# Kernel optimization log

Hardware: AMD Instinct MI355X
Metric: run time of the kernel (lower is better)

Reference implementation:

```python
import jax, jax.numpy as jnp
import numpy as np

B, T, D, NH = 4, 2048, 768, 12
DH = D // NH
NEG = -100000.0  # module uses masked_fill with -100000.0, not -inf


def setup_inputs() -> dict:
    key = jax.random.key(0)
    ks = jax.random.split(key, 9)
    s = 1.0 / np.sqrt(D)
    return {
        "x": jax.random.normal(ks[0], (B, T, D), jnp.float32),
        "wq": jax.random.normal(ks[1], (D, D), jnp.float32) * s,
        "bq": jax.random.normal(ks[2], (D,), jnp.float32) * 0.02,
        "wk": jax.random.normal(ks[3], (D, D), jnp.float32) * s,
        "bk": jax.random.normal(ks[4], (D,), jnp.float32) * 0.02,
        "wv": jax.random.normal(ks[5], (D, D), jnp.float32) * s,
        "bv": jax.random.normal(ks[6], (D,), jnp.float32) * 0.02,
        "wo": jax.random.normal(ks[7], (D, D), jnp.float32) * s,
        "bo": jax.random.normal(ks[8], (D,), jnp.float32) * 0.02,
    }


def reference(x, wq, bq, wk, bk, wv, bv, wo, bo):
    Bx, Tx, E = x.shape
    # torch Linear: y = x @ W.T + b, weight shape [out, in]
    def heads(w, b):
        return (x @ w.T + b).reshape(Bx, Tx, NH, DH).transpose(0, 2, 1, 3)  # [B,nh,T,dh]
    Q, K, V = heads(wq, bq), heads(wk, bk), heads(wv, bv)
    scale = 1.0 / jnp.sqrt(jnp.float32(DH))
    QK = jnp.einsum("bhqd,bhkd->bhqk", Q, K) * scale  # [B,nh,T,T]
    causal = jnp.tril(jnp.ones((Tx, Tx), dtype=bool))
    QK = jnp.where(causal, QK, NEG)
    A = jax.nn.softmax(QK, axis=-1)  # attn_dropout p=0 (eval)
    Z = jnp.einsum("bhqk,bhkd->bhqd", A, V)
    Z = Z.transpose(0, 2, 1, 3).reshape(Bx, Tx, E)
    return Z @ wo.T + bo  # resid_dropout p=0 (eval)
```

## Files before the change

kernel.cpp:

```cpp
#include <hip/hip_runtime.h>


#define B_ 4
#define T_ 2048
#define D_ 768
#define NH_ 12
#define DH_ 64
#define M_ (B_ * T_)

typedef __attribute__((ext_vector_type(8))) short bf16x8;
typedef __attribute__((ext_vector_type(4))) float f32x4;

__device__ __forceinline__ unsigned short f2bf(float f) {
  unsigned int u = __builtin_bit_cast(unsigned int, f);
  u += 0x7FFFu + ((u >> 16) & 1u);
  return (unsigned short)(u >> 16);
}

__device__ __forceinline__ void async16(const void* g, void* l) {
  __builtin_amdgcn_global_load_lds(
      (const __attribute__((address_space(1))) unsigned int*)g,
      (__attribute__((address_space(3))) unsigned int*)l, 16, 0, 0);
}

__global__ void cvt_kernel(const float* __restrict__ x, const float* __restrict__ wq,
                           const float* __restrict__ wk, const float* __restrict__ wv,
                           const float* __restrict__ wo,
                           unsigned short* __restrict__ xb, unsigned short* __restrict__ wqb,
                           unsigned short* __restrict__ wkb, unsigned short* __restrict__ wvb,
                           unsigned short* __restrict__ wob) {
  const float* src; unsigned short* dst; int n4;
  switch (blockIdx.y) {
    case 0: src = x;  dst = xb;  n4 = M_ * D_ / 4; break;
    case 1: src = wq; dst = wqb; n4 = D_ * D_ / 4; break;
    case 2: src = wk; dst = wkb; n4 = D_ * D_ / 4; break;
    case 3: src = wv; dst = wvb; n4 = D_ * D_ / 4; break;
    default: src = wo; dst = wob; n4 = D_ * D_ / 4; break;
  }
  int stride = gridDim.x * blockDim.x;
  for (int i = blockIdx.x * blockDim.x + threadIdx.x; i < n4; i += stride) {
    float4 v = ((const float4*)src)[i];
    ushort4 o;
    o.x = f2bf(v.x); o.y = f2bf(v.y); o.z = f2bf(v.z); o.w = f2bf(v.w);
    ((ushort4*)dst)[i] = o;
  }
}

__global__ __launch_bounds__(256) void gemm_kernel(
    const unsigned short* __restrict__ A,
    const unsigned short* __restrict__ W0, const unsigned short* __restrict__ W1,
    const unsigned short* __restrict__ W2,
    const float* __restrict__ bias0, const float* __restrict__ bias1,
    const float* __restrict__ bias2,
    void* out0, void* out1, void* out2,
    float s0, float s1, float s2,
    int M, int N, int K, int qkv) {
  __shared__ __align__(16) unsigned short As[2][128 * 64];
  __shared__ __align__(16) unsigned short Bs[2][128 * 64];

  int bid = blockIdx.x;
  int xcd = bid & 7, g = bid >> 3;
  int mt, nt, y;
  if (qkv) { mt = xcd + ((g / 18) << 3); int sub = g % 18; y = sub / 6; nt = sub % 6; }
  else     { mt = xcd + ((g / 6) << 3);  nt = g % 6; y = 0; }

  const unsigned short* W = y == 0 ? W0 : (y == 1 ? W1 : W2);
  const float* bias = y == 0 ? bias0 : (y == 1 ? bias1 : bias2);
  void* outp = y == 0 ? out0 : (y == 1 ? out1 : out2);
  float scl = y == 0 ? s0 : (y == 1 ? s1 : s2);
  int mode = qkv ? ((y == 2) ? 2 : 1) : 0;

  int tid = threadIdx.x, lane = tid & 63, w = tid >> 6;
  int l15 = lane & 15, l4 = lane >> 4;
  int wr = w >> 1, wc = w & 1;

  int m0 = mt << 7;
  int n0 = nt << 7;

  f32x4 acc[4][4] = {};

  int sRow[4], sCol[4];
#pragma unroll
  for (int c = 0; c < 4; ++c) {
    int pos = ((c * 4 + w) * 64 + lane) * 8;
    int row = pos >> 6, colE = pos & 63;
    sRow[c] = row;
    sCol[c] = colE ^ ((row & 7) << 3);
  }

#pragma unroll
  for (int c = 0; c < 4; ++c) {
    async16(A + (size_t)(m0 + sRow[c]) * K + sCol[c], (char*)As[0] + (c * 4 + w) * 1024);
    async16(W + (size_t)(n0 + sRow[c]) * K + sCol[c], (char*)Bs[0] + (c * 4 + w) * 1024);
  }

  int nkt = K >> 6;
#pragma unroll 1
  for (int t = 0; t < nkt; ++t) {
    int cur = t & 1;
    __syncthreads();
    if (t + 1 < nkt) {
      int kt1 = (t + 1) << 6;
#pragma unroll
      for (int c = 0; c < 4; ++c) {
        async16(A + (size_t)(m0 + sRow[c]) * K + kt1 + sCol[c],
                (char*)As[cur ^ 1] + (c * 4 + w) * 1024);
        async16(W + (size_t)(n0 + sRow[c]) * K + kt1 + sCol[c],
                (char*)Bs[cur ^ 1] + (c * 4 + w) * 1024);
      }
    }
#pragma unroll
    for (int ks = 0; ks < 2; ++ks) {
      bf16x8 af[4], bfr[4];
#pragma unroll
      for (int m = 0; m < 4; ++m) {
        int row = wr * 64 + m * 16 + l15;
        int cb = (ks * 64 + l4 * 16) ^ ((row & 7) << 4);
        af[m] = *(const bf16x8*)((const char*)As[cur] + row * 128 + cb);
      }
#pragma unroll
      for (int n = 0; n < 4; ++n) {
        int row = wc * 64 + n * 16 + l15;
        int cb = (ks * 64 + l4 * 16) ^ ((row & 7) << 4);
        bfr[n] = *(const bf16x8*)((const char*)Bs[cur] + row * 128 + cb);
      }
#pragma unroll
      for (int m = 0; m < 4; ++m)
#pragma unroll
        for (int n = 0; n < 4; ++n)
          acc[m][n] = __builtin_amdgcn_mfma_f32_16x16x32_bf16(af[m], bfr[n], acc[m][n], 0, 0, 0);
    }
  }

  if (mode == 2) {
#pragma unroll
    for (int n = 0; n < 4; ++n) {
      int col = n0 + wc * 64 + n * 16 + l15;
      float bv = bias[col];
      int h = col >> 6, d = col & 63;
#pragma unroll
      for (int m = 0; m < 4; ++m) {
        int rbase = m0 + wr * 64 + m * 16 + l4 * 4;
        int bb = rbase >> 11, t = rbase & (T_ - 1);
        ushort4 o;
        o.x = f2bf(acc[m][n][0] + bv);
        o.y = f2bf(acc[m][n][1] + bv);
        o.z = f2bf(acc[m][n][2] + bv);
        o.w = f2bf(acc[m][n][3] + bv);
        *(ushort4*)((unsigned short*)outp + ((size_t)(bb * NH_ + h) * DH_ + d) * T_ + t) = o;
      }
    }
  } else {
#pragma unroll
    for (int n = 0; n < 4; ++n) {
      int col = n0 + wc * 64 + n * 16 + l15;
      float bv = bias[col];
#pragma unroll
      for (int m = 0; m < 4; ++m) {
        int rbase = m0 + wr * 64 + m * 16 + l4 * 4;
#pragma unroll
        for (int r = 0; r < 4; ++r) {
          float v = (acc[m][n][r] + bv) * scl;
          size_t idx = (size_t)(rbase + r) * N + col;
          if (mode == 1) ((unsigned short*)outp)[idx] = f2bf(v);
          else           ((float*)outp)[idx] = v;
        }
      }
    }
  }
}

__global__ __launch_bounds__(256, 3) void attn_kernel(
    const unsigned short* __restrict__ Q, const unsigned short* __restrict__ Kg,
    const unsigned short* __restrict__ VT, unsigned short* __restrict__ Z) {
  __shared__ __align__(16) char lds[41984];

  int tid = threadIdx.x, lane = tid & 63, w = tid >> 6;
  int l15 = lane & 15, l4 = lane >> 4;
  int bid = blockIdx.x;
  int xcd = bid & 7, g = bid >> 3;
  int bh = xcd + ((g >> 4) << 3);
  int pr = g & 15;
  int b = bh / NH_, h = bh % NH_;

  const unsigned short* Qb = Q + (size_t)(b * T_) * D_ + h * DH_;
  const unsigned short* Kb = Kg + (size_t)(b * T_) * D_ + h * DH_;
  const unsigned short* VTb = VT + (size_t)(b * NH_ + h) * DH_ * T_;

  int sRow[2], sCol[2];
#pragma unroll
  for (int c = 0; c < 2; ++c) {
    int pos = ((c * 4 + w) * 64 + lane) * 8;
    int row = pos >> 6, colE = pos & 63;
    sRow[c] = row;
    sCol[c] = colE ^ ((row & 7) << 3);
  }

  int koff[4][2];
#pragma unroll
  for (int nt = 0; nt < 4; ++nt)
#pragma unroll
    for (int ks = 0; ks < 2; ++ks) {
      int row = nt * 16 + l15;
      koff[nt][ks] = row * 128 + ((ks * 64 + l4 * 16) ^ ((row & 7) << 4));
    }
  char* pw_wr = lds + 32768 + w * 2304 + l15 * 144 + l4 * 8;
  const char* pw_rd = lds + 32768 + w * 2304 + l15 * 144 + l4 * 16;

#define ATTN_TILE(KCUR, VCUR, KNXT, VNXT)                                              \
  do {                                                                                 \
    __syncthreads();          \
    if (t + 1 < ntiles) {                                                              \
      int kv1 = (t + 1) * 64;                                                          \
      _Pragma("unroll") for (int c = 0; c < 2; ++c) {                                  \
        async16(Kb + (size_t)(kv1 + sRow[c]) * D_ + sCol[c],                           \
                lds + KNXT + (c * 4 + w) * 1024);                                      \
        async16(VTb + (size_t)sRow[c] * T_ + kv1 + sCol[c],                            \
                lds + VNXT + (c * 4 + w) * 1024);                                      \
      }                                                                                \
    }                                                                                  \
    f32x4 st[4];                                                                       \
    _Pragma("unroll") for (int nt = 0; nt < 4; ++nt) {                                 \
      f32x4 a = {};                                                                    \
      a = __builtin_amdgcn_mfma_f32_16x16x32_bf16(                                     \
          *(const bf16x8*)(lds + KCUR + koff[nt][0]), qf0, a, 0, 0, 0);                \
      a = __builtin_amdgcn_mfma_f32_16x16x32_bf16(                                     \
          *(const bf16x8*)(lds + KCUR + koff[nt][1]), qf1, a, 0, 0, 0);                \
      st[nt] = a;                                                                      \
    }                                                                                  \
    if (t == qt) {                                  \
      int kv0 = t * 64;                                                                \
      _Pragma("unroll") for (int nt = 0; nt < 4; ++nt)                                 \
        _Pragma("unroll") for (int r = 0; r < 4; ++r) {                                \
          int kv = kv0 + nt * 16 + l4 * 4 + r;                                         \
          if (kv > qrow) st[nt][r] = -1e30f;                                           \
        }                                                                              \
    }                                                                                  \
    _Pragma("unroll") for (int nt = 0; nt < 4; ++nt) {                                 \
      float u0 = __builtin_amdgcn_exp2f(st[nt][0]);                                    \
      float u1 = __builtin_amdgcn_exp2f(st[nt][1]);                                    \
      float u2 = __builtin_amdgcn_exp2f(st[nt][2]);                                    \
      float u3 = __builtin_amdgcn_exp2f(st[nt][3]);                                    \
      l_run += (u0 + u1) + (u2 + u3);                                                  \
      uint2 o;                                                                         \
      asm("v_cvt_pk_bf16_f32 %0, %1, %2" : "=v"(o.x) : "v"(u0), "v"(u1));              \
      asm("v_cvt_pk_bf16_f32 %0, %1, %2" : "=v"(o.y) : "v"(u2), "v"(u3));              \
      *(uint2*)(pw_wr + nt * 32) = o;                                                  \
    }                                                                                  \
    {                                                                                  \
      bf16x8 pb0 = *(const bf16x8*)(pw_rd + 0);                                        \
      bf16x8 pb1 = *(const bf16x8*)(pw_rd + 64);                                       \
      _Pragma("unroll") for (int dt = 0; dt < 4; ++dt) {                               \
        bf16x8 vf0 = *(const bf16x8*)(lds + VCUR + koff[dt][0]);                       \
        bf16x8 vf1 = *(const bf16x8*)(lds + VCUR + koff[dt][1]);                       \
        zt[dt] = __builtin_amdgcn_mfma_f32_16x16x32_bf16(vf0, pb0, zt[dt], 0, 0, 0);   \
        zt[dt] = __builtin_amdgcn_mfma_f32_16x16x32_bf16(vf1, pb1, zt[dt], 0, 0, 0);   \
      }                                                                                \
    }                                                                                  \
  } while (0)

#pragma unroll 1
  for (int pass = 0; pass < 2; ++pass) {
    int qt = pass == 0 ? (31 - pr) : pr;
    int q0 = qt * 64;
    int qrow = q0 + w * 16 + l15;

    bf16x8 qf0, qf1;
    {
      const unsigned short* qp = Qb + (size_t)qrow * D_ + l4 * 8;
      qf0 = *(const bf16x8*)qp;
      qf1 = *(const bf16x8*)(qp + 32);
    }

    f32x4 zt[4] = {};
    float l_run = 0.f;
    int ntiles = qt + 1;

    __syncthreads();
#pragma unroll
    for (int c = 0; c < 2; ++c) {
      async16(Kb + (size_t)sRow[c] * D_ + sCol[c], lds + 0 + (c * 4 + w) * 1024);
      async16(VTb + (size_t)sRow[c] * T_ + sCol[c], lds + 16384 + (c * 4 + w) * 1024);
    }

#pragma unroll 1
    for (int t = 0; t < ntiles; ++t) {
      if ((t & 1) == 0) {
        ATTN_TILE(0, 16384, 8192, 24576);
      } else {
        ATTN_TILE(8192, 24576, 0, 16384);
      }
    }

    float l = l_run;
    l += __shfl_xor(l, 16);
    l += __shfl_xor(l, 32);
    float inv = __builtin_amdgcn_rcpf(l);
    unsigned short* Zrow = Z + (size_t)(b * T_ + qrow) * D_ + h * DH_;
#pragma unroll
    for (int dt = 0; dt < 4; ++dt) {
      ushort4 o;
      o.x = f2bf(zt[dt][0] * inv);
      o.y = f2bf(zt[dt][1] * inv);
      o.z = f2bf(zt[dt][2] * inv);
      o.w = f2bf(zt[dt][3] * inv);
      *(ushort4*)(Zrow + dt * 16 + l4 * 4) = o;
    }
  }
#undef ATTN_TILE
}

extern "C" void kernel_launch(void* const* d_in, const int* in_sizes, int n_in,
                              void* d_out, int out_size, void* d_ws, size_t ws_size,
                              hipStream_t stream) {
  (void)in_sizes; (void)n_in; (void)out_size; (void)ws_size;
  const float* x  = (const float*)d_in[0];
  const float* wq = (const float*)d_in[1];
  const float* bq = (const float*)d_in[2];
  const float* wk = (const float*)d_in[3];
  const float* bk = (const float*)d_in[4];
  const float* wv = (const float*)d_in[5];
  const float* bv = (const float*)d_in[6];
  const float* wo = (const float*)d_in[7];
  const float* bo = (const float*)d_in[8];

  char* ws = (char*)d_ws;
  const size_t XB = (size_t)M_ * D_ * 2;
  const size_t WB = (size_t)D_ * D_ * 2;
  unsigned short* xb  = (unsigned short*)(ws);
  unsigned short* wqb = (unsigned short*)(ws + XB);
  unsigned short* wkb = (unsigned short*)(ws + XB + WB);
  unsigned short* wvb = (unsigned short*)(ws + XB + 2 * WB);
  unsigned short* wob = (unsigned short*)(ws + XB + 3 * WB);
  unsigned short* Qb  = (unsigned short*)(ws + XB + 4 * WB);
  unsigned short* Kb  = (unsigned short*)(ws + XB + 4 * WB + XB);
  unsigned short* VTb = (unsigned short*)(ws + XB + 4 * WB + 2 * XB);
  unsigned short* Zb  = xb;

  const float SCALE_Q = 0.125f * 1.44269504f;

  cvt_kernel<<<dim3(1024, 5), 256, 0, stream>>>(x, wq, wk, wv, wo, xb, wqb, wkb, wvb, wob);
  gemm_kernel<<<dim3(8 * 8 * 18), 256, 0, stream>>>(
      xb, wqb, wkb, wvb, bq, bk, bv, Qb, Kb, VTb, SCALE_Q, 1.0f, 1.0f, M_, D_, D_, 1);
  attn_kernel<<<dim3(8 * 6 * 16), 256, 0, stream>>>(Qb, Kb, VTb, Zb);
  gemm_kernel<<<dim3(8 * 8 * 6), 256, 0, stream>>>(
      Zb, wob, wob, wob, bo, bo, bo, d_out, d_out, d_out, 1.0f, 1.0f, 1.0f, M_, D_, D_, 0);
}
```

Baseline: 126.6 us.

## Switch attention to 32x32x16 MFMA with register-resident P and 128-row query tiles

After: 121.8 us. 1.04x faster.

```diff
diff --git a/kernel.cpp b/kernel.cpp
--- a/kernel.cpp
+++ b/kernel.cpp
@@ -10,6 +10,8 @@
 
 typedef __attribute__((ext_vector_type(8))) short bf16x8;
 typedef __attribute__((ext_vector_type(4))) float f32x4;
+typedef __attribute__((ext_vector_type(16))) float f32x16;
+typedef __attribute__((ext_vector_type(4))) unsigned int u32x4;
 
 __device__ __forceinline__ unsigned short f2bf(float f) {
   unsigned int u = __builtin_bit_cast(unsigned int, f);
@@ -170,22 +172,29 @@
   }
 }
 
-__global__ __launch_bounds__(256, 3) void attn_kernel(
+__global__ __launch_bounds__(256, 2) void attn_kernel(
     const unsigned short* __restrict__ Q, const unsigned short* __restrict__ Kg,
     const unsigned short* __restrict__ VT, unsigned short* __restrict__ Z) {
-  __shared__ __align__(16) char lds[41984];
+  __shared__ __align__(16) char lds[57344];
 
   int tid = threadIdx.x, lane = tid & 63, w = tid >> 6;
-  int l15 = lane & 15, l4 = lane >> 4;
+  int l31 = lane & 31, hi = lane >> 5;
   int bid = blockIdx.x;
   int xcd = bid & 7, g = bid >> 3;
-  int bh = xcd + ((g >> 4) << 3);
-  int pr = g & 15;
+  int qt = 15 - g / 6;
+  int bh = xcd + (g % 6) * 8;
   int b = bh / NH_, h = bh % NH_;
+  int q0 = qt * 128;
+  int qrow = q0 + w * 32 + l31;
 
   const unsigned short* Qb = Q + (size_t)(b * T_) * D_ + h * DH_;
   const unsigned short* Kb = Kg + (size_t)(b * T_) * D_ + h * DH_;
   const unsigned short* VTb = VT + (size_t)(b * NH_ + h) * DH_ * T_;
+
+  bf16x8 qf[4];
+#pragma unroll
+  for (int s = 0; s < 4; ++s)
+    qf[s] = *(const bf16x8*)(Qb + (size_t)qrow * D_ + s * 16 + hi * 8);
 
   int sRow[2], sCol[2];
 #pragma unroll
@@ -196,16 +205,24 @@
     sCol[c] = colE ^ ((row & 7) << 3);
   }
 
-  int koff[4][2];
-#pragma unroll
-  for (int nt = 0; nt < 4; ++nt)
-#pragma unroll
-    for (int ks = 0; ks < 2; ++ks) {
-      int row = nt * 16 + l15;
-      koff[nt][ks] = row * 128 + ((ks * 64 + l4 * 16) ^ ((row & 7) << 4));
-    }
-  char* pw_wr = lds + 32768 + w * 2304 + l15 * 144 + l4 * 8;
-  const char* pw_rd = lds + 32768 + w * 2304 + l15 * 144 + l4 * 16;
+  int koff[2][4];
+#pragma unroll
+  for (int n = 0; n < 2; ++n)
+#pragma unroll
+    for (int s = 0; s < 4; ++s) {
+      int row = n * 32 + l31;
+      koff[n][s] = row * 128 + ((s * 32 + hi * 16) ^ ((row & 7) << 4));
+    }
+
+  f32x16 zt[2] = {};
+  float l_run = 0.f;
+  int ntiles = 2 * qt + 2;
+
+#pragma unroll
+  for (int c = 0; c < 2; ++c) {
+    async16(Kb + (size_t)sRow[c] * D_ + sCol[c], lds + 0 + (c * 4 + w) * 1024);
+    async16(VTb + (size_t)sRow[c] * T_ + sCol[c], lds + 16384 + (c * 4 + w) * 1024);
+  }
 
 #define ATTN_TILE(KCUR, VCUR, KNXT, VNXT)                                              \
   do {                                                                                 \
@@ -219,95 +236,79 @@
                 lds + VNXT + (c * 4 + w) * 1024);                                      \
       }                                                                                \
     }                                                                                  \
-    f32x4 st[4];                                                                       \
-    _Pragma("unroll") for (int nt = 0; nt < 4; ++nt) {                                 \
-      f32x4 a = {};                                                                    \
-      a = __builtin_amdgcn_mfma_f32_16x16x32_bf16(                                     \
-          *(const bf16x8*)(lds + KCUR + koff[nt][0]), qf0, a, 0, 0, 0);                \
-      a = __builtin_amdgcn_mfma_f32_16x16x32_bf16(                                     \
-          *(const bf16x8*)(lds + KCUR + koff[nt][1]), qf1, a, 0, 0, 0);                \
-      st[nt] = a;                                                                      \
-    }                                                                                  \
-    if (t == qt) {                                  \
-      int kv0 = t * 64;                                                                \
-      _Pragma("unroll") for (int nt = 0; nt < 4; ++nt)                                 \
-        _Pragma("unroll") for (int r = 0; r < 4; ++r) {                                \
-          int kv = kv0 + nt * 16 + l4 * 4 + r;                                         \
-          if (kv > qrow) st[nt][r] = -1e30f;                                           \
-        }                                                                              \
-    }                                                                                  \
-    _Pragma("unroll") for (int nt = 0; nt < 4; ++nt) {                                 \
-      float u0 = __builtin_amdgcn_exp2f(st[nt][0]);                                    \
-      float u1 = __builtin_amdgcn_exp2f(st[nt][1]);                                    \
-      float u2 = __builtin_amdgcn_exp2f(st[nt][2]);                                    \
-      float u3 = __builtin_amdgcn_exp2f(st[nt][3]);                                    \
-      l_run += (u0 + u1) + (u2 + u3);                                                  \
-      uint2 o;                                                                         \
-      asm("v_cvt_pk_bf16_f32 %0, %1, %2" : "=v"(o.x) : "v"(u0), "v"(u1));              \
-      asm("v_cvt_pk_bf16_f32 %0, %1, %2" : "=v"(o.y) : "v"(u2), "v"(u3));              \
-      *(uint2*)(pw_wr + nt * 32) = o;                                                  \
-    }                                                                                  \
-    {                                                                                  \
-      bf16x8 pb0 = *(const bf16x8*)(pw_rd + 0);                                        \
-      bf16x8 pb1 = *(const bf16x8*)(pw_rd + 64);                                       \
-      _Pragma("unroll") for (int dt = 0; dt < 4; ++dt) {                               \
-        bf16x8 vf0 = *(const bf16x8*)(lds + VCUR + koff[dt][0]);                       \
-        bf16x8 vf1 = *(const bf16x8*)(lds + VCUR + koff[dt][1]);                       \
-        zt[dt] = __builtin_amdgcn_mfma_f32_16x16x32_bf16(vf0, pb0, zt[dt], 0, 0, 0);   \
-        zt[dt] = __builtin_amdgcn_mfma_f32_16x16x32_bf16(vf1, pb1, zt[dt], 0, 0, 0);   \
-      }                                                                                \
-    }                                                                                  \
+    f32x16 st[2];                                                                      \
+    __builtin_amdgcn_s_setprio(1);                                                     \
+    _Pragma("unroll") for (int n = 0; n < 2; ++n) {                                    \
+      f32x16 a = {};                                                                   \
+      _Pragma("unroll") for (int s = 0; s < 4; ++s) {                                  \
+        bf16x8 kf = *(const bf16x8*)(lds + KCUR + koff[n][s]);                         \
+        a = __builtin_amdgcn_mfma_f32_32x32x16_bf16(kf, qf[s], a, 0, 0, 0);            \
+      }                                                                                \
+      st[n] = a;                                                                       \
+    }                                                                                  \
+    __builtin_amdgcn_s_setprio(0);                                                     \
+    if (t >= 2 * qt) {                            \
+      int kvb = t * 64;                                                                \
+      _Pragma("unroll") for (int n = 0; n < 2; ++n)                                    \
+        _Pragma("unroll") for (int m = 0; m < 4; ++m)                                  \
+          _Pragma("unroll") for (int c2 = 0; c2 < 4; ++c2) {                           \
+            int kv = kvb + n * 32 + m * 8 + hi * 4 + c2;                               \
+            if (kv > qrow) st[n][m * 4 + c2] = -1e30f;                                 \
+          }                                                                            \
+    }                                                                                  \
+    bf16x8 pb[4];                                                                      \
+    _Pragma("unroll") for (int n = 0; n < 2; ++n) {                                    \
+      float u[16];                                                                     \
+      _Pragma("unroll") for (int r = 0; r < 16; ++r) {                                 \
+        u[r] = __builtin_amdgcn_exp2f(st[n][r]);                                       \
+        l_run += u[r];                                                                 \
+      }                                                                                \
+      _Pragma("unroll") for (int hf = 0; hf < 2; ++hf) {                               \
+        unsigned int A0, A1, B0, B1;                                                   \
+        asm("v_cvt_pk_bf16_f32 %0, %1, %2" : "=v"(A0) : "v"(u[hf*8+0]), "v"(u[hf*8+1]));\
+        asm("v_cvt_pk_bf16_f32 %0, %1, %2" : "=v"(A1) : "v"(u[hf*8+2]), "v"(u[hf*8+3]));\
+        asm("v_cvt_pk_bf16_f32 %0, %1, %2" : "=v"(B0) : "v"(u[hf*8+4]), "v"(u[hf*8+5]));\
+        asm("v_cvt_pk_bf16_f32 %0, %1, %2" : "=v"(B1) : "v"(u[hf*8+6]), "v"(u[hf*8+7]));\
+        asm("v_permlane32_swap_b32 %0, %1" : "+v"(A0), "+v"(B0));                      \
+        asm("v_permlane32_swap_b32 %0, %1" : "+v"(A1), "+v"(B1));                      \
+        u32x4 pk; pk[0] = A0; pk[1] = A1; pk[2] = B0; pk[3] = B1;                      \
+        pb[n * 2 + hf] = __builtin_bit_cast(bf16x8, pk);                               \
+      }                                                                                \
+    }                                                                                  \
+    __builtin_amdgcn_s_setprio(1);                                                     \
+    _Pragma("unroll") for (int dt = 0; dt < 2; ++dt) {                                 \
+      _Pragma("unroll") for (int s = 0; s < 4; ++s) {                                  \
+        bf16x8 vf = *(const bf16x8*)(lds + VCUR + koff[dt][s]);                        \
+        zt[dt] = __builtin_amdgcn_mfma_f32_32x32x16_bf16(vf, pb[s], zt[dt], 0, 0, 0);  \
+      }                                                                                \
+    }                                                                                  \
+    __builtin_amdgcn_s_setprio(0);                                                     \
   } while (0)
 
 #pragma unroll 1
-  for (int pass = 0; pass < 2; ++pass) {
-    int qt = pass == 0 ? (31 - pr) : pr;
-    int q0 = qt * 64;
-    int qrow = q0 + w * 16 + l15;
-
-    bf16x8 qf0, qf1;
-    {
-      const unsigned short* qp = Qb + (size_t)qrow * D_ + l4 * 8;
-      qf0 = *(const bf16x8*)qp;
-      qf1 = *(const bf16x8*)(qp + 32);
-    }
-
-    f32x4 zt[4] = {};
-    float l_run = 0.f;
-    int ntiles = qt + 1;
-
-    __syncthreads();
-#pragma unroll
-    for (int c = 0; c < 2; ++c) {
-      async16(Kb + (size_t)sRow[c] * D_ + sCol[c], lds + 0 + (c * 4 + w) * 1024);
-      async16(VTb + (size_t)sRow[c] * T_ + sCol[c], lds + 16384 + (c * 4 + w) * 1024);
-    }
-
-#pragma unroll 1
-    for (int t = 0; t < ntiles; ++t) {
-      if ((t & 1) == 0) {
-        ATTN_TILE(0, 16384, 8192, 24576);
-      } else {
-        ATTN_TILE(8192, 24576, 0, 16384);
-      }
-    }
-
-    float l = l_run;
-    l += __shfl_xor(l, 16);
-    l += __shfl_xor(l, 32);
-    float inv = __builtin_amdgcn_rcpf(l);
-    unsigned short* Zrow = Z + (size_t)(b * T_ + qrow) * D_ + h * DH_;
-#pragma unroll
-    for (int dt = 0; dt < 4; ++dt) {
+  for (int t = 0; t < ntiles; ++t) {
+    if ((t & 1) == 0) {
+      ATTN_TILE(0, 16384, 8192, 24576);
+    } else {
+      ATTN_TILE(8192, 24576, 0, 16384);
+    }
+  }
+#undef ATTN_TILE
+
+  l_run += __shfl_xor(l_run, 32);
+  float inv = __builtin_amdgcn_rcpf(l_run);
+  unsigned short* Zrow = Z + (size_t)(b * T_ + qrow) * D_ + h * DH_;
+#pragma unroll
+  for (int dt = 0; dt < 2; ++dt)
+#pragma unroll
+    for (int m = 0; m < 4; ++m) {
       ushort4 o;
-      o.x = f2bf(zt[dt][0] * inv);
-      o.y = f2bf(zt[dt][1] * inv);
-      o.z = f2bf(zt[dt][2] * inv);
-      o.w = f2bf(zt[dt][3] * inv);
-      *(ushort4*)(Zrow + dt * 16 + l4 * 4) = o;
-    }
-  }
-#undef ATTN_TILE
+      o.x = f2bf(zt[dt][m * 4 + 0] * inv);
+      o.y = f2bf(zt[dt][m * 4 + 1] * inv);
+      o.z = f2bf(zt[dt][m * 4 + 2] * inv);
+      o.w = f2bf(zt[dt][m * 4 + 3] * inv);
+      *(ushort4*)(Zrow + dt * 32 + m * 8 + hi * 4) = o;
+    }
 }
 
 extern "C" void kernel_launch(void* const* d_in, const int* in_sizes, int n_in,
@@ -342,7 +343,7 @@
   cvt_kernel<<<dim3(1024, 5), 256, 0, stream>>>(x, wq, wk, wv, wo, xb, wqb, wkb, wvb, wob);
   gemm_kernel<<<dim3(8 * 8 * 18), 256, 0, stream>>>(
       xb, wqb, wkb, wvb, bq, bk, bv, Qb, Kb, VTb, SCALE_Q, 1.0f, 1.0f, M_, D_, D_, 1);
-  attn_kernel<<<dim3(8 * 6 * 16), 256, 0, stream>>>(Qb, Kb, VTb, Zb);
+  attn_kernel<<<dim3(768), 256, 0, stream>>>(Qb, Kb, VTb, Zb);
   gemm_kernel<<<dim3(8 * 8 * 6), 256, 0, stream>>>(
       Zb, wob, wob, wob, bo, bo, bo, d_out, d_out, d_out, 1.0f, 1.0f, 1.0f, M_, D_, D_, 0);
 }
```
